# Optimization experiments

Measured on AMD Instinct MI355X. Metric: run time of the kernel, lower is better.

The kernel has to match this reference:

```python
import jax, jax.numpy as jnp
import numpy as np

B, IN, H, M = 65536, 128, 256, 32


def setup_inputs() -> dict:
    key = jax.random.key(0)
    ks = jax.random.split(key, 8)
    s_i = 1.0 / np.sqrt(IN + H)
    s_m = 1.0 / np.sqrt(M)
    return {
        "input": jax.random.normal(ks[0], (B, IN), jnp.float32),
        "media": jax.random.normal(ks[1], (B, M), jnp.float32),
        "h_t": jax.random.normal(ks[2], (B, H), jnp.float32),
        "c_t": jax.random.normal(ks[3], (B, H), jnp.float32),
        "Wi": jax.random.normal(ks[4], (H, IN + H), jnp.float32) * s_i,
        "bi": jax.random.normal(ks[5], (H,), jnp.float32) * s_i,
        "Wm": jax.random.normal(ks[6], (H, M), jnp.float32) * s_m,
        "bm": jax.random.normal(ks[7], (H,), jnp.float32) * s_m,
    }


def reference(input, media, h_t, c_t, Wi, bi, Wm, bm):
    # original, so all gates share one pre-activation g.
    combined = jnp.concatenate([input, h_t], axis=1)
    g = combined @ Wi.T + bi                     # [B, H]
    gate = jax.nn.sigmoid(g)                     # i == f == o
    c = c_t * gate + jnp.tanh(g) * gate          # new cell state
    c_r = jnp.tanh(c)
    m = jax.nn.sigmoid(media @ Wm.T + bm)        # media gate [B, H]
    c_f = c - c_r + c_r * m
    h = jnp.tanh(c_f) * gate
    # classification=False -> output is h; returns (output, h, c)
    return (h, h, c)
```

## Files before the change

### kernel.cpp

```cpp
#include <hip/hip_runtime.h>

#define BB  65536
#define INW 128
#define HH  256
#define MM  32
#define KK  (INW + HH)
#define NKC 12

typedef __attribute__((ext_vector_type(8))) short bf16x8;
typedef __attribute__((ext_vector_type(4))) float f32x4;

#define SB() __builtin_amdgcn_sched_barrier(0)

__device__ __forceinline__ unsigned short f32_to_bf16(float f) {
    union { float f; unsigned u; } v; v.f = f;
    return (unsigned short)((v.u + 0x7fffu + ((v.u >> 16) & 1u)) >> 16);
}

__device__ __forceinline__ bf16x8 cvt8(f32x4 a, f32x4 b) {
    bf16x8 r;
    r[0] = (short)f32_to_bf16(a[0]); r[1] = (short)f32_to_bf16(a[1]);
    r[2] = (short)f32_to_bf16(a[2]); r[3] = (short)f32_to_bf16(a[3]);
    r[4] = (short)f32_to_bf16(b[0]); r[5] = (short)f32_to_bf16(b[1]);
    r[6] = (short)f32_to_bf16(b[2]); r[7] = (short)f32_to_bf16(b[3]);
    return r;
}

__device__ __forceinline__ float rcp_f(float x) { return __builtin_amdgcn_rcpf(x); }
__device__ __forceinline__ float sigmoid_f(float x) { return rcp_f(1.0f + __expf(-x)); }
__device__ __forceinline__ float tanh_f(float x) { return 1.0f - 2.0f * rcp_f(__expf(2.0f * x) + 1.0f); }

__global__ void pack_weights(const float* __restrict__ Wi, const float* __restrict__ Wm,
                             unsigned short* __restrict__ Wi_p, unsigned short* __restrict__ Wm_p) {
    int id = blockIdx.x * 256 + threadIdx.x;
    if (id < 2 * NKC * 8 * 512) {
        int blk = id >> 9;
        int e   = id & 511;
        int lane = e >> 3, j = e & 7;
        int lrow = lane & 15, quad = lane >> 4;
        int h  = blk / (NKC * 8);
        int b  = blk % (NKC * 8);
        int kc = b >> 3;
        int t  = b & 7;
        int n  = h * 128 + t * 16 + lrow;
        int k  = kc * 32 + quad * 8 + j;
        Wi_p[id] = f32_to_bf16(Wi[(size_t)n * KK + k]);
    }
    if (id < 2 * 8 * 512) {
        int blk = id >> 9;
        int e   = id & 511;
        int lane = e >> 3, j = e & 7;
        int lrow = lane & 15, quad = lane >> 4;
        int h = blk >> 3;
        int t = blk & 7;
        int n = h * 128 + t * 16 + lrow;
        Wm_p[id] = f32_to_bf16(Wm[(size_t)n * MM + quad * 8 + j]);
    }
}

__device__ __forceinline__ void epilogue4(f32x4 g4, f32x4 am, f32x4 ct4, f32x4 bi4, f32x4 bm4,
                                          float* __restrict__ p, size_t outH) {
    f32x4 h4, c4;
#pragma unroll
    for (int r = 0; r < 4; ++r) {
        float g    = g4[r] + bi4[r];
        float mp   = am[r] + bm4[r];
        float gate = sigmoid_f(g);
        float tg   = tanh_f(g);
        float c    = ct4[r] * gate + tg * gate;
        float cr   = tanh_f(c);
        float mg   = sigmoid_f(mp);
        float cf   = c - cr + cr * mg;
        float h    = tanh_f(cf) * gate;
        h4[r] = h; c4[r] = c;
    }
    __builtin_nontemporal_store(h4, (f32x4*)p);
    __builtin_nontemporal_store(h4, (f32x4*)(p + outH));
    __builtin_nontemporal_store(c4, (f32x4*)(p + 2 * outH));
}

__global__ __launch_bounds__(256, 3) void rlstm_main(
    const float* __restrict__ input, const float* __restrict__ media,
    const float* __restrict__ h_t,   const float* __restrict__ c_t,
    const unsigned short* __restrict__ Wi_p, const float* __restrict__ bi,
    const unsigned short* __restrict__ Wm_p, const float* __restrict__ bm,
    float* __restrict__ out)
{
    __shared__ unsigned short wiq[NKC * 4 * 512];
    __shared__ unsigned short wmq[4 * 512];
    __shared__ float lbi[64], lbm[64];

    const int tid  = threadIdx.x;
    const int wave = tid >> 6;
    const int lane = tid & 63;
    const int lrow = lane & 15;
    const int quad = lane >> 4;

    const int q      = blockIdx.x & 3;
    const int half   = q >> 1;
    const int thalf  = q & 1;
    const int n0q    = q * 64;
    const int rowblk = blockIdx.x >> 2;

    const int arow0 = rowblk * 128 + wave * 16 + lrow;

    f32x4 act[24];
#define ACT_PTR(arow, kc) ((kc) < 4 ? (input + (size_t)(arow) * INW + (kc) * 32 + quad * 8) \
                                    : (h_t   + (size_t)(arow) * HH  + ((kc) - 4) * 32 + quad * 8))
#define LOAD_ACTS(arow) { _Pragma("unroll") for (int kc_ = 0; kc_ < NKC; ++kc_) {            \
        const float* s_ = ACT_PTR(arow, kc_);                                                \
        act[2 * kc_]     = ((const f32x4*)s_)[0];                                            \
        act[2 * kc_ + 1] = ((const f32x4*)s_)[1]; } }

    LOAD_ACTS(arow0);
    SB();

#pragma unroll
    for (int r = 0; r < 12; ++r) {
        int le  = (r * 256 + tid) * 8;
        int kc  = le >> 11;
        int rem = le & 2047;
        bf16x8 v = *(const bf16x8*)(Wi_p + (size_t)(half * NKC + kc) * 4096 + thalf * 2048 + rem);
        *(bf16x8*)(wiq + le) = v;
    }
    {
        int le = tid * 8;
        bf16x8 v = *(const bf16x8*)(Wm_p + (size_t)half * 4096 + thalf * 2048 + le);
        *(bf16x8*)(wmq + le) = v;
    }
    if (tid < 64)        lbi[tid]      = bi[n0q + tid];
    else if (tid < 128)  lbm[tid - 64] = bm[n0q + (tid - 64)];
    __syncthreads();

    const size_t outH = (size_t)BB * HH;

#pragma unroll
    for (int tl = 0; tl < 2; ++tl) {
        const int arow = arow0 + tl * 64;
        const size_t rowbase = (size_t)arow * HH + n0q;

        f32x4 ct[4];
        SB();
#pragma unroll
        for (int t = 0; t < 4; ++t)
            ct[t] = *(const f32x4*)(c_t + rowbase + t * 16 + quad * 4);
        f32x4 md0 = *(const f32x4*)(media + (size_t)arow * MM + quad * 8);
        f32x4 md1 = *(const f32x4*)(media + (size_t)arow * MM + quad * 8 + 4);
        SB();

        f32x4 acc[4];
#pragma unroll
        for (int t = 0; t < 4; ++t) acc[t] = (f32x4){0.f, 0.f, 0.f, 0.f};
#pragma unroll
        for (int kc = 0; kc < NKC; ++kc) {
            bf16x8 xa = cvt8(act[2 * kc], act[2 * kc + 1]);
#pragma unroll
            for (int t = 0; t < 4; ++t) {
                bf16x8 wf = *(const bf16x8*)(wiq + kc * 2048 + t * 512 + lane * 8);
                acc[t] = __builtin_amdgcn_mfma_f32_16x16x32_bf16(wf, xa, acc[t], 0, 0, 0);
            }
        }
        SB();
        if (tl == 0) { LOAD_ACTS(arow0 + 64); }
        SB();

        bf16x8 mf = cvt8(md0, md1);
#pragma unroll
        for (int t = 0; t < 4; ++t) {
            bf16x8 wmf = *(const bf16x8*)(wmq + t * 512 + lane * 8);
            f32x4 am = __builtin_amdgcn_mfma_f32_16x16x32_bf16(
                wmf, mf, (f32x4){0.f, 0.f, 0.f, 0.f}, 0, 0, 0);
            const int nb = t * 16 + quad * 4;
            f32x4 bi4 = *(const f32x4*)(lbi + nb);
            f32x4 bm4 = *(const f32x4*)(lbm + nb);
            epilogue4(acc[t], am, ct[t], bi4, bm4, out + rowbase + nb, outH);
        }
        SB();
    }
#undef ACT_PTR
#undef LOAD_ACTS
}

extern "C" void kernel_launch(void* const* d_in, const int* in_sizes, int n_in,
                              void* d_out, int out_size, void* d_ws, size_t ws_size,
                              hipStream_t stream) {
    const float* input = (const float*)d_in[0];
    const float* media = (const float*)d_in[1];
    const float* h_t   = (const float*)d_in[2];
    const float* c_t   = (const float*)d_in[3];
    const float* Wi    = (const float*)d_in[4];
    const float* bi    = (const float*)d_in[5];
    const float* Wm    = (const float*)d_in[6];
    const float* bm    = (const float*)d_in[7];
    float* out = (float*)d_out;

    unsigned short* Wi_p = (unsigned short*)d_ws;
    unsigned short* Wm_p = Wi_p + 2 * NKC * 8 * 512;

    hipLaunchKernelGGL(pack_weights, dim3((2 * NKC * 8 * 512 + 255) / 256), dim3(256), 0, stream,
                       Wi, Wm, Wi_p, Wm_p);
    hipLaunchKernelGGL(rlstm_main, dim3(512 * 4), dim3(256), 0, stream,
                       input, media, h_t, c_t, Wi_p, bi, Wm_p, bm, out);
}
```

Measured before the change: 369.9 us.

## Prefetch activations via inline-asm loads, swizzle block order, lower occupancy bound

```diff
diff --git a/kernel.cpp b/kernel.cpp
--- a/kernel.cpp
+++ b/kernel.cpp
@@ -11,6 +11,8 @@
 typedef __attribute__((ext_vector_type(4))) float f32x4;
 
 #define SB() __builtin_amdgcn_sched_barrier(0)
+#define GL4(dst, ptr) asm volatile("global_load_dwordx4 %0, %1, off" : "=v"(dst) : "v"(ptr) : "memory")
+#define WAITV0() do { asm volatile("s_waitcnt vmcnt(0)" ::: "memory"); __builtin_amdgcn_sched_barrier(0); } while (0)
 
 __device__ __forceinline__ unsigned short f32_to_bf16(float f) {
     union { float f; unsigned u; } v; v.f = f;
@@ -79,7 +81,7 @@
     __builtin_nontemporal_store(c4, (f32x4*)(p + 2 * outH));
 }
 
-__global__ __launch_bounds__(256, 3) void rlstm_main(
+__global__ __launch_bounds__(256, 2) void rlstm_main(
     const float* __restrict__ input, const float* __restrict__ media,
     const float* __restrict__ h_t,   const float* __restrict__ c_t,
     const unsigned short* __restrict__ Wi_p, const float* __restrict__ bi,
@@ -96,24 +98,31 @@
     const int lrow = lane & 15;
     const int quad = lane >> 4;
 
-    const int q      = blockIdx.x & 3;
+    const int bid = blockIdx.x;
+    const int vid = (bid & 7) * 256 + (bid >> 3);
+    const int q      = vid & 3;
+    const int rowblk = vid >> 2;
     const int half   = q >> 1;
     const int thalf  = q & 1;
     const int n0q    = q * 64;
-    const int rowblk = blockIdx.x >> 2;
 
     const int arow0 = rowblk * 128 + wave * 16 + lrow;
-
-    f32x4 act[24];
-#define ACT_PTR(arow, kc) ((kc) < 4 ? (input + (size_t)(arow) * INW + (kc) * 32 + quad * 8) \
-                                    : (h_t   + (size_t)(arow) * HH  + ((kc) - 4) * 32 + quad * 8))
-#define LOAD_ACTS(arow) { _Pragma("unroll") for (int kc_ = 0; kc_ < NKC; ++kc_) {            \
-        const float* s_ = ACT_PTR(arow, kc_);                                                \
-        act[2 * kc_]     = ((const f32x4*)s_)[0];                                            \
-        act[2 * kc_ + 1] = ((const f32x4*)s_)[1]; } }
-
-    LOAD_ACTS(arow0);
-    SB();
+    const int arow1 = arow0 + 64;
+    const size_t rb0 = (size_t)arow0 * HH + n0q;
+    const size_t rb1 = (size_t)arow1 * HH + n0q;
+
+    f32x4 a[24], ct0[4], md00, md01;
+#pragma unroll
+    for (int kc = 0; kc < NKC; ++kc) {
+        const float* s = (kc < 4) ? input + (size_t)arow0 * INW + kc * 32 + quad * 8
+                                  : h_t   + (size_t)arow0 * HH  + (kc - 4) * 32 + quad * 8;
+        GL4(a[2 * kc], s);
+        GL4(a[2 * kc + 1], s + 4);
+    }
+#pragma unroll
+    for (int t = 0; t < 4; ++t) GL4(ct0[t], c_t + rb0 + t * 16 + quad * 4);
+    GL4(md00, media + (size_t)arow0 * MM + quad * 8);
+    GL4(md01, media + (size_t)arow0 * MM + quad * 8 + 4);
 
 #pragma unroll
     for (int r = 0; r < 12; ++r) {
@@ -130,41 +139,41 @@
     }
     if (tid < 64)        lbi[tid]      = bi[n0q + tid];
     else if (tid < 128)  lbm[tid - 64] = bm[n0q + (tid - 64)];
+    WAITV0();
     __syncthreads();
 
     const size_t outH = (size_t)BB * HH;
 
-#pragma unroll
-    for (int tl = 0; tl < 2; ++tl) {
-        const int arow = arow0 + tl * 64;
-        const size_t rowbase = (size_t)arow * HH + n0q;
-
-        f32x4 ct[4];
-        SB();
-#pragma unroll
-        for (int t = 0; t < 4; ++t)
-            ct[t] = *(const f32x4*)(c_t + rowbase + t * 16 + quad * 4);
-        f32x4 md0 = *(const f32x4*)(media + (size_t)arow * MM + quad * 8);
-        f32x4 md1 = *(const f32x4*)(media + (size_t)arow * MM + quad * 8 + 4);
-        SB();
-
-        f32x4 acc[4];
-#pragma unroll
-        for (int t = 0; t < 4; ++t) acc[t] = (f32x4){0.f, 0.f, 0.f, 0.f};
-#pragma unroll
-        for (int kc = 0; kc < NKC; ++kc) {
-            bf16x8 xa = cvt8(act[2 * kc], act[2 * kc + 1]);
-#pragma unroll
-            for (int t = 0; t < 4; ++t) {
-                bf16x8 wf = *(const bf16x8*)(wiq + kc * 2048 + t * 512 + lane * 8);
-                acc[t] = __builtin_amdgcn_mfma_f32_16x16x32_bf16(wf, xa, acc[t], 0, 0, 0);
-            }
-        }
-        SB();
-        if (tl == 0) { LOAD_ACTS(arow0 + 64); }
-        SB();
-
-        bf16x8 mf = cvt8(md0, md1);
+    f32x4 acc[4];
+#pragma unroll
+    for (int t = 0; t < 4; ++t) acc[t] = (f32x4){0.f, 0.f, 0.f, 0.f};
+#pragma unroll
+    for (int kc = 0; kc < NKC; ++kc) {
+        bf16x8 xa = cvt8(a[2 * kc], a[2 * kc + 1]);
+#pragma unroll
+        for (int t = 0; t < 4; ++t) {
+            bf16x8 wf = *(const bf16x8*)(wiq + kc * 2048 + t * 512 + lane * 8);
+            acc[t] = __builtin_amdgcn_mfma_f32_16x16x32_bf16(wf, xa, acc[t], 0, 0, 0);
+        }
+    }
+    SB();
+
+    f32x4 ct1[4], md10, md11;
+#pragma unroll
+    for (int kc = 0; kc < NKC; ++kc) {
+        const float* s = (kc < 4) ? input + (size_t)arow1 * INW + kc * 32 + quad * 8
+                                  : h_t   + (size_t)arow1 * HH  + (kc - 4) * 32 + quad * 8;
+        GL4(a[2 * kc], s);
+        GL4(a[2 * kc + 1], s + 4);
+    }
+#pragma unroll
+    for (int t = 0; t < 4; ++t) GL4(ct1[t], c_t + rb1 + t * 16 + quad * 4);
+    GL4(md10, media + (size_t)arow1 * MM + quad * 8);
+    GL4(md11, media + (size_t)arow1 * MM + quad * 8 + 4);
+    SB();
+
+    {
+        bf16x8 mf = cvt8(md00, md01);
 #pragma unroll
         for (int t = 0; t < 4; ++t) {
             bf16x8 wmf = *(const bf16x8*)(wmq + t * 512 + lane * 8);
@@ -173,12 +182,35 @@
             const int nb = t * 16 + quad * 4;
             f32x4 bi4 = *(const f32x4*)(lbi + nb);
             f32x4 bm4 = *(const f32x4*)(lbm + nb);
-            epilogue4(acc[t], am, ct[t], bi4, bm4, out + rowbase + nb, outH);
-        }
-        SB();
-    }
-#undef ACT_PTR
-#undef LOAD_ACTS
+            epilogue4(acc[t], am, ct0[t], bi4, bm4, out + rb0 + nb, outH);
+        }
+    }
+
+    WAITV0();
+#pragma unroll
+    for (int t = 0; t < 4; ++t) acc[t] = (f32x4){0.f, 0.f, 0.f, 0.f};
+#pragma unroll
+    for (int kc = 0; kc < NKC; ++kc) {
+        bf16x8 xa = cvt8(a[2 * kc], a[2 * kc + 1]);
+#pragma unroll
+        for (int t = 0; t < 4; ++t) {
+            bf16x8 wf = *(const bf16x8*)(wiq + kc * 2048 + t * 512 + lane * 8);
+            acc[t] = __builtin_amdgcn_mfma_f32_16x16x32_bf16(wf, xa, acc[t], 0, 0, 0);
+        }
+    }
+    {
+        bf16x8 mf = cvt8(md10, md11);
+#pragma unroll
+        for (int t = 0; t < 4; ++t) {
+            bf16x8 wmf = *(const bf16x8*)(wmq + t * 512 + lane * 8);
+            f32x4 am = __builtin_amdgcn_mfma_f32_16x16x32_bf16(
+                wmf, mf, (f32x4){0.f, 0.f, 0.f, 0.f}, 0, 0, 0);
+            const int nb = t * 16 + quad * 4;
+            f32x4 bi4 = *(const f32x4*)(lbi + nb);
+            f32x4 bm4 = *(const f32x4*)(lbm + nb);
+            epilogue4(acc[t], am, ct1[t], bi4, bm4, out + rb1 + nb, outH);
+        }
+    }
 }
 
 extern "C" void kernel_launch(void* const* d_in, const int* in_sizes, int n_in,
```

Result: no change. 376.9 us (+1.9%).

## Loop each 512-thread block over four row tiles, reusing staged weights

Applied to the files above, without the earlier changes.

```diff
diff --git a/kernel.cpp b/kernel.cpp
--- a/kernel.cpp
+++ b/kernel.cpp
@@ -9,8 +9,6 @@
 
 typedef __attribute__((ext_vector_type(8))) short bf16x8;
 typedef __attribute__((ext_vector_type(4))) float f32x4;
-
-#define SB() __builtin_amdgcn_sched_barrier(0)
 
 __device__ __forceinline__ unsigned short f32_to_bf16(float f) {
     union { float f; unsigned u; } v; v.f = f;
@@ -79,7 +77,7 @@
     __builtin_nontemporal_store(c4, (f32x4*)(p + 2 * outH));
 }
 
-__global__ __launch_bounds__(256, 3) void rlstm_main(
+__global__ __launch_bounds__(512, 4) void rlstm_main(
     const float* __restrict__ input, const float* __restrict__ media,
     const float* __restrict__ h_t,   const float* __restrict__ c_t,
     const unsigned short* __restrict__ Wi_p, const float* __restrict__ bi,
@@ -96,37 +94,27 @@
     const int lrow = lane & 15;
     const int quad = lane >> 4;
 
-    const int q      = blockIdx.x & 3;
-    const int half   = q >> 1;
-    const int thalf  = q & 1;
-    const int n0q    = q * 64;
-    const int rowblk = blockIdx.x >> 2;
-
-    const int arow0 = rowblk * 128 + wave * 16 + lrow;
-
-    f32x4 act[24];
-#define ACT_PTR(arow, kc) ((kc) < 4 ? (input + (size_t)(arow) * INW + (kc) * 32 + quad * 8) \
-                                    : (h_t   + (size_t)(arow) * HH  + ((kc) - 4) * 32 + quad * 8))
-#define LOAD_ACTS(arow) { _Pragma("unroll") for (int kc_ = 0; kc_ < NKC; ++kc_) {            \
-        const float* s_ = ACT_PTR(arow, kc_);                                                \
-        act[2 * kc_]     = ((const f32x4*)s_)[0];                                            \
-        act[2 * kc_ + 1] = ((const f32x4*)s_)[1]; } }
-
-    LOAD_ACTS(arow0);
-    SB();
+    const int b = blockIdx.x;
+    const int k = b & 7;
+    const int j = b >> 3;
+    const int q = j & 3;
+    const int g = j >> 2;
+    const int half  = q >> 1;
+    const int thalf = q & 1;
+    const int n0q   = q * 64;
 
 #pragma unroll
-    for (int r = 0; r < 12; ++r) {
-        int le  = (r * 256 + tid) * 8;
+    for (int r = 0; r < 6; ++r) {
+        int le  = (r * 512 + tid) * 8;
         int kc  = le >> 11;
         int rem = le & 2047;
-        bf16x8 v = *(const bf16x8*)(Wi_p + (size_t)(half * NKC + kc) * 4096 + thalf * 2048 + rem);
-        *(bf16x8*)(wiq + le) = v;
+        *(bf16x8*)(wiq + le) =
+            *(const bf16x8*)(Wi_p + (size_t)(half * NKC + kc) * 4096 + thalf * 2048 + rem);
     }
-    {
+    if (tid < 256) {
         int le = tid * 8;
-        bf16x8 v = *(const bf16x8*)(Wm_p + (size_t)half * 4096 + thalf * 2048 + le);
-        *(bf16x8*)(wmq + le) = v;
+        *(bf16x8*)(wmq + le) =
+            *(const bf16x8*)(Wm_p + (size_t)half * 4096 + thalf * 2048 + le);
     }
     if (tid < 64)        lbi[tid]      = bi[n0q + tid];
     else if (tid < 128)  lbm[tid - 64] = bm[n0q + (tid - 64)];
@@ -135,34 +123,38 @@
     const size_t outH = (size_t)BB * HH;
 
 #pragma unroll
-    for (int tl = 0; tl < 2; ++tl) {
-        const int arow = arow0 + tl * 64;
-        const size_t rowbase = (size_t)arow * HH + n0q;
+    for (int it = 0; it < 4; ++it) {
+        const int rowblk = k * 64 + g * 4 + it;
+        const int arow   = rowblk * 128 + wave * 16 + lrow;
+        const size_t rb  = (size_t)arow * HH + n0q;
 
+        f32x4 a[24];
+#pragma unroll
+        for (int kc = 0; kc < NKC; ++kc) {
+            const float* s = (kc < 4) ? input + (size_t)arow * INW + kc * 32 + quad * 8
+                                      : h_t   + (size_t)arow * HH  + (kc - 4) * 32 + quad * 8;
+            a[2 * kc]     = ((const f32x4*)s)[0];
+            a[2 * kc + 1] = ((const f32x4*)s)[1];
+        }
         f32x4 ct[4];
-        SB();
 #pragma unroll
         for (int t = 0; t < 4; ++t)
-            ct[t] = *(const f32x4*)(c_t + rowbase + t * 16 + quad * 4);
+            ct[t] = *(const f32x4*)(c_t + rb + t * 16 + quad * 4);
         f32x4 md0 = *(const f32x4*)(media + (size_t)arow * MM + quad * 8);
         f32x4 md1 = *(const f32x4*)(media + (size_t)arow * MM + quad * 8 + 4);
-        SB();
 
         f32x4 acc[4];
 #pragma unroll
         for (int t = 0; t < 4; ++t) acc[t] = (f32x4){0.f, 0.f, 0.f, 0.f};
 #pragma unroll
         for (int kc = 0; kc < NKC; ++kc) {
-            bf16x8 xa = cvt8(act[2 * kc], act[2 * kc + 1]);
+            bf16x8 xa = cvt8(a[2 * kc], a[2 * kc + 1]);
 #pragma unroll
             for (int t = 0; t < 4; ++t) {
                 bf16x8 wf = *(const bf16x8*)(wiq + kc * 2048 + t * 512 + lane * 8);
                 acc[t] = __builtin_amdgcn_mfma_f32_16x16x32_bf16(wf, xa, acc[t], 0, 0, 0);
             }
         }
-        SB();
-        if (tl == 0) { LOAD_ACTS(arow0 + 64); }
-        SB();
 
         bf16x8 mf = cvt8(md0, md1);
 #pragma unroll
@@ -173,12 +165,9 @@
             const int nb = t * 16 + quad * 4;
             f32x4 bi4 = *(const f32x4*)(lbi + nb);
             f32x4 bm4 = *(const f32x4*)(lbm + nb);
-            epilogue4(acc[t], am, ct[t], bi4, bm4, out + rowbase + nb, outH);
+            epilogue4(acc[t], am, ct[t], bi4, bm4, out + rb + nb, outH);
         }
-        SB();
     }
-#undef ACT_PTR
-#undef LOAD_ACTS
 }
 
 extern "C" void kernel_launch(void* const* d_in, const int* in_sizes, int n_in,
@@ -199,6 +188,6 @@
 
     hipLaunchKernelGGL(pack_weights, dim3((2 * NKC * 8 * 512 + 255) / 256), dim3(256), 0, stream,
                        Wi, Wm, Wi_p, Wm_p);
-    hipLaunchKernelGGL(rlstm_main, dim3(512 * 4), dim3(256), 0, stream,
+    hipLaunchKernelGGL(rlstm_main, dim3(512), dim3(512), 0, stream,
                        input, media, h_t, c_t, Wi_p, bi, Wm_p, bm, out);
 }
```

After: 378.6 us. +2.4%, slower.
